# Optimization experiments

Measured on AMD Instinct MI355X. Metric: run time of the kernel, lower is better.

## Reference

```python
import jax, jax.numpy as jnp
import numpy as np

N_NODES = 100000
N_EDGES = 1600000
N_FEAT = 128
HIDDEN = 128
N_CLASSES = 40
MAX_DEPTH = 4
INIT_TEMP = 1.0  # temperature (non-trainable)
N_AGGR = 3       # ['mean', 'max', 'self']


def setup_inputs() -> dict:
    key = jax.random.key(0)
    ks = jax.random.split(key, 16)
    s = 1.0 / np.sqrt(HIDDEN)
    inp = {
        'x': jax.random.normal(ks[0], (N_NODES, N_FEAT), dtype=jnp.float32),
        'edge_index': jax.random.randint(ks[1], (2, N_EDGES), 0, N_NODES, dtype=jnp.int32),
        'W_pre': jax.random.normal(ks[2], (N_FEAT, HIDDEN), dtype=jnp.float32) / np.sqrt(N_FEAT),
        'b_pre': jnp.zeros((HIDDEN,), dtype=jnp.float32),
        'W_depth': jax.random.normal(ks[3], (HIDDEN, 2), dtype=jnp.float32) * s,
        'b_depth': jnp.zeros((2,), dtype=jnp.float32),
        'W_aggr': jax.random.normal(ks[4], (HIDDEN, N_AGGR), dtype=jnp.float32) * s,
        'b_aggr': jnp.zeros((N_AGGR,), dtype=jnp.float32),
        'W_conv': jax.random.normal(ks[5], (MAX_DEPTH, HIDDEN, HIDDEN), dtype=jnp.float32) * s,
        'b_conv': jnp.zeros((MAX_DEPTH, HIDDEN), dtype=jnp.float32),
        'W_post': jax.random.normal(ks[6], (HIDDEN, N_CLASSES), dtype=jnp.float32) * s,
        'b_post': jnp.zeros((N_CLASSES,), dtype=jnp.float32),
    }
    return inp


def _mix_aggr_conv(x, src, dst, deg, W, b, aggr_w):
    # MixAggrConvLayer: transform then per-node convex mix of {mean, max, self}
    h = x @ W + b                                   # [N, H]
    msg = h[src]                                    # [E, H] gather
    mean_a = jax.ops.segment_sum(msg, dst, num_segments=N_NODES) / deg[:, None]
    max_a = jax.ops.segment_max(msg, dst, num_segments=N_NODES)
    max_a = jnp.where(jnp.isfinite(max_a), max_a, 0.0)  # isolated nodes -> 0
    return aggr_w[:, 0:1] * mean_a + aggr_w[:, 1:2] * max_a + aggr_w[:, 2:3] * h


def reference(x, edge_index, W_pre, b_pre, W_depth, b_depth, W_aggr, b_aggr,
              W_conv, b_conv, W_post, b_post):
    src, dst = edge_index[0], edge_index[1]
    deg = jnp.maximum(
        jax.ops.segment_sum(jnp.ones((src.shape[0],), jnp.float32), dst,
                            num_segments=N_NODES), 1.0)

    # pre_mp + (Dropout eval = identity) + ReLU
    h = jax.nn.relu(x @ W_pre + b_pre)              # [N, H]

    continue_pr = jnp.ones((N_NODES,), jnp.float32)
    selected = jnp.zeros((N_NODES, HIDDEN), jnp.float32)
    for i in range(MAX_DEPTH):
        hd = jax.lax.stop_gradient(h)               # controllers see detached x
        stop_prob = jax.nn.softmax((hd @ W_depth + b_depth) / INIT_TEMP, axis=-1)
        aggr_prob = jax.nn.softmax((hd @ W_aggr + b_aggr) / INIT_TEMP, axis=-1)
        h = _mix_aggr_conv(h, src, dst, deg, W_conv[i], b_conv[i], aggr_prob)
        h = jax.nn.relu(h)                          # dropout (eval) + relu
        selected = selected + (continue_pr * stop_prob[:, 1])[:, None] * h
        continue_pr = continue_pr * stop_prob[:, 0]

    logits = selected @ W_post + b_post             # [N, C]
    return jax.nn.log_softmax(logits, axis=1)
```

## Files before the change

### kernel.cpp

```cpp
#include <hip/hip_runtime.h>
#include <math.h>

#define HIDDEN 128
#define NCLS 40
#define BMAX 1024

typedef __attribute__((ext_vector_type(8))) short short8;
typedef __attribute__((ext_vector_type(4))) float f32x4;
typedef __attribute__((ext_vector_type(2))) float f32x2;

__device__ __forceinline__ unsigned short f2bf(float f) {
    unsigned u = __float_as_uint(f);
    unsigned r = u + 0x7FFFu + ((u >> 16) & 1u);
    return (unsigned short)(r >> 16);
}
__device__ __forceinline__ float bf_lo(unsigned u) { return __uint_as_float(u << 16); }
__device__ __forceinline__ float bf_hi(unsigned u) { return __uint_as_float(u & 0xFFFF0000u); }

__global__ void k_wprep(const float* __restrict__ Wp, const float* __restrict__ Wc,
                        const float* __restrict__ Wd, const float* __restrict__ Wa,
                        unsigned short* __restrict__ WpreT, unsigned short* __restrict__ WT) {
    int i = blockIdx.x * 256 + threadIdx.x;
    if (i < 16384) {
        int n = i >> 7, k = i & 127;
        WpreT[i] = f2bf(Wp[k * 128 + n]);
    } else if (i < 16384 + 4 * 18432) {
        int j = i - 16384;
        int d = j / 18432;
        int rem = j % 18432;
        int n = rem >> 7, k = rem & 127;
        float v = 0.f;
        if (n < 128)      v = Wc[d * 16384 + k * 128 + n];
        else if (n < 130) v = Wd[k * 2 + (n - 128)];
        else if (n < 133) v = Wa[k * 3 + (n - 130)];
        WT[j] = f2bf(v);
    }
}


__launch_bounds__(256)
__global__ void k_bcount(const int* __restrict__ ei, int E, int* __restrict__ bucket_cnt) {
    __shared__ int hist[BMAX];
    const int tid = threadIdx.x;
    for (int i = tid; i < BMAX; i += 256) hist[i] = 0;
    __syncthreads();
    const int e0 = blockIdx.x * 4096;
    #pragma unroll
    for (int i = 0; i < 16; i++) {
        int e = e0 + i * 256 + tid;
        if (e < E) atomicAdd(&hist[ei[E + e] >> 8], 1);
    }
    __syncthreads();
    for (int i = tid; i < BMAX; i += 256) {
        int v = hist[i];
        if (v > 0) atomicAdd(&bucket_cnt[i], v);
    }
}

__global__ void k_bscan(const int* __restrict__ bucket_cnt, int nb,
                        int* __restrict__ bucket_base, int* __restrict__ bucket_cursor) {
    __shared__ int sd[256];
    const int tid = threadIdx.x;
    int v[4];
    int sum = 0;
    #pragma unroll
    for (int j = 0; j < 4; j++) {
        int b = tid * 4 + j;
        v[j] = (b < nb) ? bucket_cnt[b] : 0;
        sum += v[j];
    }
    sd[tid] = sum;
    __syncthreads();
    #pragma unroll
    for (int off = 1; off < 256; off <<= 1) {
        int t = (tid >= off) ? sd[tid - off] : 0;
        __syncthreads();
        sd[tid] += t;
        __syncthreads();
    }
    int base = sd[tid] - sum;
    #pragma unroll
    for (int j = 0; j < 4; j++) {
        int b = tid * 4 + j;
        if (b < nb) {
            bucket_base[b] = base;
            bucket_cursor[b] = base;
            base += v[j];
        }
    }
}

__launch_bounds__(256)
__global__ void k_bin(const int* __restrict__ ei, int E,
                      int* __restrict__ bucket_cursor, unsigned* __restrict__ binned) {
    __shared__ int hist[BMAX];
    __shared__ int rankc[BMAX];
    __shared__ int lbase[BMAX];
    const int tid = threadIdx.x;
    const int e0 = blockIdx.x * 4096;
    for (int i = tid; i < BMAX; i += 256) { hist[i] = 0; rankc[i] = 0; }
    __syncthreads();
    int bkt[16];
    unsigned pk[16];
    #pragma unroll
    for (int i = 0; i < 16; i++) {
        int e = e0 + i * 256 + tid;
        if (e < E) {
            int s = ei[e];
            int d = ei[E + e];
            bkt[i] = d >> 8;
            pk[i] = ((unsigned)(d & 255) << 24) | (unsigned)s;
            atomicAdd(&hist[bkt[i]], 1);
        } else bkt[i] = -1;
    }
    __syncthreads();
    for (int i = tid; i < BMAX; i += 256)
        if (hist[i] > 0) lbase[i] = atomicAdd(&bucket_cursor[i], hist[i]);
    __syncthreads();
    #pragma unroll
    for (int i = 0; i < 16; i++) {
        if (bkt[i] >= 0) {
            int r = atomicAdd(&rankc[bkt[i]], 1);
            binned[lbase[bkt[i]] + r] = pk[i];
        }
    }
}

__launch_bounds__(256)
__global__ void k_scatter(const unsigned* __restrict__ binned,
                          const int* __restrict__ bucket_base,
                          const int* __restrict__ bucket_cnt,
                          int* __restrict__ row_start,
                          int* __restrict__ csr_off, int N) {
    __shared__ int hist[256];
    __shared__ int rs[256];
    __shared__ int cur[256];
    const int tid = threadIdx.x;
    hist[tid] = 0;
    __syncthreads();
    const int base = bucket_base[blockIdx.x];
    const int cnt = bucket_cnt[blockIdx.x];
    for (int i = tid; i < cnt; i += 256)
        atomicAdd(&hist[binned[base + i] >> 24], 1);
    __syncthreads();
    int v = hist[tid];
    rs[tid] = v;
    __syncthreads();
    #pragma unroll
    for (int off = 1; off < 256; off <<= 1) {
        int t = (tid >= off) ? rs[tid - off] : 0;
        __syncthreads();
        rs[tid] += t;
        __syncthreads();
    }
    int gstart = base + rs[tid] - v;
    int n = (blockIdx.x << 8) + tid;
    if (n < N) {
        row_start[n] = gstart;
        if (n == N - 1) row_start[N] = gstart + v;
    }
    __syncthreads();
    rs[tid] = gstart;
    cur[tid] = 0;
    __syncthreads();
    for (int i = tid; i < cnt; i += 256) {
        unsigned p = binned[base + i];
        int dl = (int)(p >> 24);
        int r = atomicAdd(&cur[dl], 1);
        csr_off[rs[dl] + r] = (int)((p & 0xFFFFFFu) << 7);
    }
}


template <bool AF32, bool CTRL>
__launch_bounds__(256)
__global__ void k_gemm_mfma(const void* __restrict__ Ain,
                            const unsigned short* __restrict__ Wt,
                            const float* __restrict__ bias,
                            unsigned short* __restrict__ Cb,
                            unsigned char* __restrict__ C8,
                            float* __restrict__ ctrl,
                            int M, int do_relu) {
    __shared__ unsigned short Ws[144 * 132];
    const int tid = threadIdx.x;
    const int lane = tid & 63;
    const int wv = tid >> 6;
    const int row_blk = blockIdx.x * 128;
    const int rows0 = wv * 32;
    const int l15 = lane & 15;
    const int q = lane >> 4;
    const int RWS = CTRL ? 144 : 128;

    for (int c = tid; c < RWS * 16; c += 256) {
        int r = c >> 4, ch = c & 15;
        *(uint4*)&Ws[r * 132 + ch * 8] = *(const uint4*)(Wt + (size_t)r * HIDDEN + ch * 8);
    }
    __syncthreads();

    f32x4 acc[2][8] = {};
    f32x4 acc5[2] = {};
    for (int k0 = 0; k0 < 128; k0 += 32) {
        short8 af[2];
        #pragma unroll
        for (int mi = 0; mi < 2; mi++) {
            int ar = row_blk + rows0 + mi * 16 + l15;
            if (AF32) {
                const float* A = (const float*)Ain;
                float4 v0 = make_float4(0.f, 0.f, 0.f, 0.f);
                float4 v1 = make_float4(0.f, 0.f, 0.f, 0.f);
                if (ar < M) {
                    v0 = *(const float4*)(A + (size_t)ar * HIDDEN + k0 + q * 8);
                    v1 = *(const float4*)(A + (size_t)ar * HIDDEN + k0 + q * 8 + 4);
                }
                short8 t;
                t[0] = (short)f2bf(v0.x); t[1] = (short)f2bf(v0.y);
                t[2] = (short)f2bf(v0.z); t[3] = (short)f2bf(v0.w);
                t[4] = (short)f2bf(v1.x); t[5] = (short)f2bf(v1.y);
                t[6] = (short)f2bf(v1.z); t[7] = (short)f2bf(v1.w);
                af[mi] = t;
            } else {
                const unsigned short* A = (const unsigned short*)Ain;
                short8 t = {};
                if (ar < M) t = *(const short8*)(A + (size_t)ar * HIDDEN + k0 + q * 8);
                af[mi] = t;
            }
        }
        #pragma unroll
        for (int ni = 0; ni < 8; ni++) {
            short8 bw = *(const short8*)&Ws[(ni * 16 + l15) * 132 + k0 + q * 8];
            #pragma unroll
            for (int mi = 0; mi < 2; mi++)
                acc[mi][ni] = __builtin_amdgcn_mfma_f32_16x16x32_bf16(
                    bw, af[mi], acc[mi][ni], 0, 0, 0);
        }
        if (CTRL) {
            short8 bc = *(const short8*)&Ws[(128 + l15) * 132 + k0 + q * 8];
            #pragma unroll
            for (int mi = 0; mi < 2; mi++)
                acc5[mi] = __builtin_amdgcn_mfma_f32_16x16x32_bf16(
                    bc, af[mi], acc5[mi], 0, 0, 0);
        }
    }
    #pragma unroll
    for (int mi = 0; mi < 2; mi++) {
        int node = row_blk + rows0 + mi * 16 + l15;
        if (node < M) {
            #pragma unroll
            for (int ni = 0; ni < 8; ni++) {
                int fb = ni * 16 + q * 4;
                float4 bv = *(const float4*)&bias[fb];
                float o0 = acc[mi][ni][0] + bv.x;
                float o1 = acc[mi][ni][1] + bv.y;
                float o2 = acc[mi][ni][2] + bv.z;
                float o3 = acc[mi][ni][3] + bv.w;
                if (do_relu) {
                    o0 = fmaxf(o0, 0.f); o1 = fmaxf(o1, 0.f);
                    o2 = fmaxf(o2, 0.f); o3 = fmaxf(o3, 0.f);
                }
                unsigned plo, phi;
                asm("v_cvt_pk_bf16_f32 %0, %1, %2" : "=v"(plo) : "v"(o0), "v"(o1));
                asm("v_cvt_pk_bf16_f32 %0, %1, %2" : "=v"(phi) : "v"(o2), "v"(o3));
                uint2 ov;
                ov.x = plo; ov.y = phi;
                *(uint2*)(Cb + (size_t)node * HIDDEN + fb) = ov;
                if (CTRL) {
                    unsigned w8 = 0;
                    w8 = __builtin_amdgcn_cvt_pk_fp8_f32(o0, o1, w8, 0);
                    w8 = __builtin_amdgcn_cvt_pk_fp8_f32(o2, o3, w8, 1);
                    *(unsigned*)(C8 + (size_t)node * HIDDEN + fb) = w8;
                }
            }
            if (CTRL) {
                if (q == 0) {
                    *(float4*)(ctrl + (size_t)node * 8) =
                        make_float4(acc5[mi][0], acc5[mi][1], acc5[mi][2], acc5[mi][3]);
                } else if (q == 1) {
                    ctrl[(size_t)node * 8 + 4] = acc5[mi][0];
                }
            }
        }
    }
}


#define LDE(K, JJ)                                                            \
    unsigned u##K = *(const unsigned short*)(                                 \
        ht8 + (unsigned)__builtin_amdgcn_readlane(soff, (JJ) + K) + lane2);
#define ACE(K)                                                                \
    { f32x2 p_ = __builtin_amdgcn_cvt_pk_f32_fp8(u##K, 0);                    \
      sacc += p_;                                                             \
      mx0 = fmaxf(mx0, p_.x); mx1 = fmaxf(mx1, p_.y); }

__launch_bounds__(256)
__global__ void k_depth(const unsigned char* __restrict__ ht8,
                        const unsigned short* __restrict__ ht,
                        unsigned short* __restrict__ h_out,
                        float* __restrict__ cp, float* __restrict__ wsel,
                        const float* __restrict__ ctrl,
                        const int* __restrict__ row_start,
                        const int* __restrict__ csr_off,
                        const float* __restrict__ bd, const float* __restrict__ ba,
                        int N, int first) {
    const int lane = threadIdx.x & 63;
    const int wave = threadIdx.x >> 6;
    const int node = blockIdx.x * 4 + wave;
    if (node >= N) return;
    const int nodeu = __builtin_amdgcn_readfirstlane(node);
    const int lane2 = lane << 1;

    const int start = row_start[nodeu];
    const int cnt = row_start[nodeu + 1] - start;

    int soff = (lane < cnt) ? csr_off[start + lane] : 0;
    unsigned su = *(const unsigned*)((const char*)ht + ((size_t)nodeu << 8) + (lane << 2));
    float4 c4 = *(const float4*)(ctrl + (size_t)nodeu * 8);
    float cl4 = ctrl[(size_t)nodeu * 8 + 4];

    float d0 = c4.x + bd[0], d1 = c4.y + bd[1];
    float a0 = c4.z + ba[0], a1 = c4.w + ba[1], a2 = cl4 + ba[2];
    float m2 = fmaxf(d0, d1);
    float e0 = __expf(d0 - m2), e1 = __expf(d1 - m2);
    float inv2 = __builtin_amdgcn_rcpf(e0 + e1);
    float sp0 = e0 * inv2, sp1 = e1 * inv2;
    float m3 = fmaxf(fmaxf(a0, a1), a2);
    float f0 = __expf(a0 - m3), f1 = __expf(a1 - m3), f2 = __expf(a2 - m3);
    float inv3 = __builtin_amdgcn_rcpf(f0 + f1 + f2);
    float ap0 = f0 * inv3, ap1 = f1 * inv3, ap2 = f2 * inv3;

    f32x2 sacc = {0.f, 0.f};
    float mx0 = -3.4e38f, mx1 = -3.4e38f;

    for (int eb = 0; eb < cnt; eb += 64) {
        if (eb) {
            int i2 = eb + lane;
            soff = (i2 < cnt) ? csr_off[start + i2] : 0;
        }
        int lim = min(64, cnt - eb);
        int j = 0;
        for (; j + 16 <= lim; j += 16) {
            LDE(0, j)  LDE(1, j)  LDE(2, j)  LDE(3, j)
            LDE(4, j)  LDE(5, j)  LDE(6, j)  LDE(7, j)
            LDE(8, j)  LDE(9, j)  LDE(10, j) LDE(11, j)
            LDE(12, j) LDE(13, j) LDE(14, j) LDE(15, j)
            ACE(0)  ACE(1)  ACE(2)  ACE(3)
            ACE(4)  ACE(5)  ACE(6)  ACE(7)
            ACE(8)  ACE(9)  ACE(10) ACE(11)
            ACE(12) ACE(13) ACE(14) ACE(15)
        }
        if (j + 8 <= lim) {
            LDE(0, j) LDE(1, j) LDE(2, j) LDE(3, j)
            LDE(4, j) LDE(5, j) LDE(6, j) LDE(7, j)
            ACE(0) ACE(1) ACE(2) ACE(3)
            ACE(4) ACE(5) ACE(6) ACE(7)
            j += 8;
        }
        if (j + 4 <= lim) {
            LDE(0, j) LDE(1, j) LDE(2, j) LDE(3, j)
            ACE(0) ACE(1) ACE(2) ACE(3)
            j += 4;
        }
        for (; j < lim; j++) {
            LDE(0, j)
            ACE(0)
        }
    }

    if (cnt == 0) { mx0 = 0.f; mx1 = 0.f; }
    float invd = __builtin_amdgcn_rcpf(fmaxf((float)cnt, 1.0f));
    float h0 = ap0 * (sacc.x * invd) + ap1 * mx0 + ap2 * bf_lo(su);
    float h1 = ap0 * (sacc.y * invd) + ap1 * mx1 + ap2 * bf_hi(su);
    h0 = fmaxf(h0, 0.f);
    h1 = fmaxf(h1, 0.f);
    unsigned po = ((unsigned)f2bf(h1) << 16) | (unsigned)f2bf(h0);
    *(unsigned*)((char*)h_out + ((size_t)nodeu << 8) + (lane << 2)) = po;

    if (lane == 0) {
        float cpv = first ? 1.0f : cp[nodeu];
        wsel[nodeu] = cpv * sp1;
        cp[nodeu] = cpv * sp0;
    }
}


__launch_bounds__(256)
__global__ void k_post(const unsigned short* __restrict__ h_all, size_t hstride,
                       const float* __restrict__ wsel, int N,
                       const float* __restrict__ Wp, const float* __restrict__ bp,
                       float* __restrict__ out) {
    __shared__ float Ss[32][132];
    __shared__ float Wt[NCLS][132];
    __shared__ float bs[NCLS];
    const int tid = threadIdx.x;
    const int n0 = blockIdx.x * 32;

    for (int i = tid; i < (HIDDEN * NCLS) / 4; i += 256) {
        float4 v = *(const float4*)&Wp[i * 4];
        int f = i * 4;
        int k = f / NCLS, c = f % NCLS;
        float e[4] = {v.x, v.y, v.z, v.w};
        #pragma unroll
        for (int j = 0; j < 4; j++) {
            int cc = c + j, kk = k;
            if (cc >= NCLS) { cc -= NCLS; kk++; }
            Wt[cc][kk] = e[j];
        }
    }
    if (tid < NCLS) bs[tid] = bp[tid];

    const int node_l = tid >> 3;
    const int kc = (tid & 7) * 16;
    const int ng = n0 + node_l;
    float sel[16];
    #pragma unroll
    for (int i = 0; i < 16; i++) sel[i] = 0.f;
    if (ng < N) {
        #pragma unroll
        for (int d = 0; d < 4; d++) {
            float w = wsel[(size_t)d * N + ng];
            const unsigned short* hrow = h_all + (size_t)(d + 1) * hstride + (size_t)ng * HIDDEN;
            #pragma unroll
            for (int u = 0; u < 2; u++) {
                uint4 p = *(const uint4*)(hrow + kc + u * 8);
                unsigned vs[4] = {p.x, p.y, p.z, p.w};
                #pragma unroll
                for (int j = 0; j < 4; j++) {
                    sel[u * 8 + j * 2 + 0] += w * bf_lo(vs[j]);
                    sel[u * 8 + j * 2 + 1] += w * bf_hi(vs[j]);
                }
            }
        }
    }
    #pragma unroll
    for (int u = 0; u < 4; u++)
        *(float4*)&Ss[node_l][kc + u * 4] =
            make_float4(sel[u * 4], sel[u * 4 + 1], sel[u * 4 + 2], sel[u * 4 + 3]);
    __syncthreads();

    const int c0 = (tid & 7) * 5;
    float z[5];
    #pragma unroll
    for (int i = 0; i < 5; i++) z[i] = bs[c0 + i];
    for (int k = 0; k < HIDDEN; k += 4) {
        float4 s4 = *(const float4*)&Ss[node_l][k];
        #pragma unroll
        for (int i = 0; i < 5; i++) {
            float4 w4 = *(const float4*)&Wt[c0 + i][k];
            z[i] += s4.x * w4.x + s4.y * w4.y + s4.z * w4.z + s4.w * w4.w;
        }
    }
    float m = z[0];
    #pragma unroll
    for (int i = 1; i < 5; i++) m = fmaxf(m, z[i]);
    #pragma unroll
    for (int off = 1; off < 8; off <<= 1) m = fmaxf(m, __shfl_xor(m, off));
    float s = 0.f;
    #pragma unroll
    for (int i = 0; i < 5; i++) s += expf(z[i] - m);
    #pragma unroll
    for (int off = 1; off < 8; off <<= 1) s += __shfl_xor(s, off);
    float lg = m + logf(s);
    if (ng < N) {
        #pragma unroll
        for (int i = 0; i < 5; i++)
            out[(size_t)ng * NCLS + c0 + i] = z[i] - lg;
    }
}


extern "C" void kernel_launch(void* const* d_in, const int* in_sizes, int n_in,
                              void* d_out, int out_size, void* d_ws, size_t ws_size,
                              hipStream_t stream) {
    const float* x      = (const float*)d_in[0];
    const int*   ei     = (const int*)d_in[1];
    const float* W_pre  = (const float*)d_in[2];
    const float* b_pre  = (const float*)d_in[3];
    const float* W_dep  = (const float*)d_in[4];
    const float* b_dep  = (const float*)d_in[5];
    const float* W_aggr = (const float*)d_in[6];
    const float* b_aggr = (const float*)d_in[7];
    const float* W_conv = (const float*)d_in[8];
    const float* b_conv = (const float*)d_in[9];
    const float* W_post = (const float*)d_in[10];
    const float* b_post = (const float*)d_in[11];

    const int N = in_sizes[0] / HIDDEN;
    const int E = in_sizes[1] / 2;
    const int nbuckets = (N + 255) >> 8;

    char* ws = (char*)d_ws;
    size_t off = 0;
    auto alloc = [&](size_t bytes) -> void* {
        void* p = ws + off;
        off += (bytes + 255) & ~(size_t)255;
        return p;
    };
    const size_t hstride = (size_t)N * HIDDEN;
    unsigned short* h_all  = (unsigned short*)alloc(5 * hstride * 2);
    unsigned short* ht     = (unsigned short*)alloc(hstride * 2);
    unsigned char*  ht8    = (unsigned char*)alloc(hstride);
    float* cp       = (float*)alloc((size_t)N * 4);
    float* wsel     = (float*)alloc((size_t)4 * N * 4);
    float* ctrl     = (float*)alloc((size_t)N * 8 * 4);
    unsigned short* WpreT = (unsigned short*)alloc(128 * 128 * 2);
    unsigned short* WT    = (unsigned short*)alloc(4 * 144 * 128 * 2);
    int*   row_start= (int*)alloc((size_t)(N + 8) * 4);
    int*   bucket_cnt    = (int*)alloc(BMAX * 4);
    int*   bucket_base   = (int*)alloc(BMAX * 4);
    int*   bucket_cursor = (int*)alloc(BMAX * 4);
    int*   csr_off  = (int*)alloc((size_t)E * 4);
    unsigned* binned = (unsigned*)alloc((size_t)E * 4);

    hipMemsetAsync(bucket_cnt, 0, BMAX * 4, stream);

    int ebb = (E + 4095) / 4096;
    k_bcount<<<ebb, 256, 0, stream>>>(ei, E, bucket_cnt);
    k_bscan<<<1, 256, 0, stream>>>(bucket_cnt, nbuckets, bucket_base, bucket_cursor);
    k_bin<<<ebb, 256, 0, stream>>>(ei, E, bucket_cursor, binned);
    k_scatter<<<nbuckets, 256, 0, stream>>>(binned, bucket_base, bucket_cnt,
                                            row_start, csr_off, N);

    int wtot = 16384 + 4 * 18432;
    k_wprep<<<(wtot + 255) / 256, 256, 0, stream>>>(W_pre, W_conv, W_dep, W_aggr,
                                                    WpreT, WT);

    int gblk = (N + 127) / 128;
    k_gemm_mfma<true, false><<<gblk, 256, 0, stream>>>(x, WpreT, b_pre, h_all,
                                                       nullptr, nullptr, N, 1);

    int nb4 = (N + 3) / 4;
    for (int d = 0; d < 4; d++) {
        unsigned short* h_d  = h_all + (size_t)d * hstride;
        unsigned short* h_n  = h_all + (size_t)(d + 1) * hstride;
        k_gemm_mfma<false, true><<<gblk, 256, 0, stream>>>(h_d, WT + (size_t)d * 18432,
                                                           b_conv + (size_t)d * HIDDEN,
                                                           ht, ht8, ctrl, N, 0);
        k_depth<<<nb4, 256, 0, stream>>>(ht8, ht, h_n, cp, wsel + (size_t)d * N, ctrl,
                                         row_start, csr_off,
                                         b_dep, b_aggr, N, d == 0 ? 1 : 0);
    }
    k_post<<<(N + 31) / 32, 256, 0, stream>>>(h_all, hstride, wsel, N,
                                              W_post, b_post, (float*)d_out);
}
```

Measured before the change: 528.1 us.

## Split wave into two half-waves gathering 4 fp8 features per lane

The edge-gather loop in k_depth now has each half-wave handle a different neighbour edge, with each lane loading 4 fp8 features (32-bit) instead of 2 (16-bit). This halves the number of load instructions per edge and widens each memory access. Partial sums and maxes are then merged across halves with xor-32 shuffles. It also uses the hardware v_cvt_pk_bf16_f32 instruction for the bf16 output conversion, and only the lower half-wave writes the result.

```diff
diff --git a/kernel.cpp b/kernel.cpp
--- a/kernel.cpp
+++ b/kernel.cpp
@@ -283,13 +283,16 @@
 }
 
 
-#define LDE(K, JJ)                                                            \
-    unsigned u##K = *(const unsigned short*)(                                 \
-        ht8 + (unsigned)__builtin_amdgcn_readlane(soff, (JJ) + K) + lane2);
-#define ACE(K)                                                                \
-    { f32x2 p_ = __builtin_amdgcn_cvt_pk_f32_fp8(u##K, 0);                    \
-      sacc += p_;                                                             \
-      mx0 = fmaxf(mx0, p_.x); mx1 = fmaxf(mx1, p_.y); }
+#define LDP(K, JJ)                                                            \
+    int sa##K = __builtin_amdgcn_readlane(soff, (JJ) + 2 * K);                \
+    int sb##K = __builtin_amdgcn_readlane(soff, (JJ) + 2 * K + 1);            \
+    unsigned u##K = *(const unsigned*)(ht8 + (unsigned)(half ? sb##K : sa##K) + fb4);
+#define ACP(K)                                                                \
+    { f32x2 plo_ = __builtin_amdgcn_cvt_pk_f32_fp8(u##K, 0);                  \
+      f32x2 phi_ = __builtin_amdgcn_cvt_pk_f32_fp8(u##K, 1);                  \
+      s01 += plo_; s23 += phi_;                                               \
+      mx0 = fmaxf(mx0, plo_.x); mx1 = fmaxf(mx1, plo_.y);                     \
+      mx2 = fmaxf(mx2, phi_.x); mx3 = fmaxf(mx3, phi_.y); }
 
 __launch_bounds__(256)
 __global__ void k_depth(const unsigned char* __restrict__ ht8,
@@ -306,13 +309,14 @@
     const int node = blockIdx.x * 4 + wave;
     if (node >= N) return;
     const int nodeu = __builtin_amdgcn_readfirstlane(node);
-    const int lane2 = lane << 1;
+    const int half = lane >> 5;
+    const unsigned fb4 = (unsigned)((lane & 31) << 2);
 
     const int start = row_start[nodeu];
     const int cnt = row_start[nodeu + 1] - start;
 
     int soff = (lane < cnt) ? csr_off[start + lane] : 0;
-    unsigned su = *(const unsigned*)((const char*)ht + ((size_t)nodeu << 8) + (lane << 2));
+    uint2 su = *(const uint2*)((const char*)ht + ((size_t)nodeu << 8) + ((lane & 31) << 3));
     float4 c4 = *(const float4*)(ctrl + (size_t)nodeu * 8);
     float cl4 = ctrl[(size_t)nodeu * 8 + 4];
 
@@ -327,8 +331,8 @@
     float inv3 = __builtin_amdgcn_rcpf(f0 + f1 + f2);
     float ap0 = f0 * inv3, ap1 = f1 * inv3, ap2 = f2 * inv3;
 
-    f32x2 sacc = {0.f, 0.f};
-    float mx0 = -3.4e38f, mx1 = -3.4e38f;
+    f32x2 s01 = {0.f, 0.f}, s23 = {0.f, 0.f};
+    float mx0 = -3.4e38f, mx1 = -3.4e38f, mx2 = -3.4e38f, mx3 = -3.4e38f;
 
     for (int eb = 0; eb < cnt; eb += 64) {
         if (eb) {
@@ -338,42 +342,59 @@
         int lim = min(64, cnt - eb);
         int j = 0;
         for (; j + 16 <= lim; j += 16) {
-            LDE(0, j)  LDE(1, j)  LDE(2, j)  LDE(3, j)
-            LDE(4, j)  LDE(5, j)  LDE(6, j)  LDE(7, j)
-            LDE(8, j)  LDE(9, j)  LDE(10, j) LDE(11, j)
-            LDE(12, j) LDE(13, j) LDE(14, j) LDE(15, j)
-            ACE(0)  ACE(1)  ACE(2)  ACE(3)
-            ACE(4)  ACE(5)  ACE(6)  ACE(7)
-            ACE(8)  ACE(9)  ACE(10) ACE(11)
-            ACE(12) ACE(13) ACE(14) ACE(15)
+            LDP(0, j) LDP(1, j) LDP(2, j) LDP(3, j)
+            LDP(4, j) LDP(5, j) LDP(6, j) LDP(7, j)
+            ACP(0) ACP(1) ACP(2) ACP(3)
+            ACP(4) ACP(5) ACP(6) ACP(7)
         }
         if (j + 8 <= lim) {
-            LDE(0, j) LDE(1, j) LDE(2, j) LDE(3, j)
-            LDE(4, j) LDE(5, j) LDE(6, j) LDE(7, j)
-            ACE(0) ACE(1) ACE(2) ACE(3)
-            ACE(4) ACE(5) ACE(6) ACE(7)
+            LDP(0, j) LDP(1, j) LDP(2, j) LDP(3, j)
+            ACP(0) ACP(1) ACP(2) ACP(3)
             j += 8;
         }
         if (j + 4 <= lim) {
-            LDE(0, j) LDE(1, j) LDE(2, j) LDE(3, j)
-            ACE(0) ACE(1) ACE(2) ACE(3)
+            LDP(0, j) LDP(1, j)
+            ACP(0) ACP(1)
             j += 4;
         }
-        for (; j < lim; j++) {
-            LDE(0, j)
-            ACE(0)
-        }
-    }
-
-    if (cnt == 0) { mx0 = 0.f; mx1 = 0.f; }
+        if (j + 2 <= lim) {
+            LDP(0, j)
+            ACP(0)
+            j += 2;
+        }
+        if (j < lim) {
+            int sa = __builtin_amdgcn_readlane(soff, j);
+            if (half == 0) {
+                unsigned u = *(const unsigned*)(ht8 + (unsigned)sa + fb4);
+                f32x2 plo_ = __builtin_amdgcn_cvt_pk_f32_fp8(u, 0);
+                f32x2 phi_ = __builtin_amdgcn_cvt_pk_f32_fp8(u, 1);
+                s01 += plo_; s23 += phi_;
+                mx0 = fmaxf(mx0, plo_.x); mx1 = fmaxf(mx1, plo_.y);
+                mx2 = fmaxf(mx2, phi_.x); mx3 = fmaxf(mx3, phi_.y);
+            }
+        }
+    }
+
+    s01.x += __shfl_xor(s01.x, 32); s01.y += __shfl_xor(s01.y, 32);
+    s23.x += __shfl_xor(s23.x, 32); s23.y += __shfl_xor(s23.y, 32);
+    mx0 = fmaxf(mx0, __shfl_xor(mx0, 32)); mx1 = fmaxf(mx1, __shfl_xor(mx1, 32));
+    mx2 = fmaxf(mx2, __shfl_xor(mx2, 32)); mx3 = fmaxf(mx3, __shfl_xor(mx3, 32));
+
+    if (cnt == 0) { mx0 = 0.f; mx1 = 0.f; mx2 = 0.f; mx3 = 0.f; }
     float invd = __builtin_amdgcn_rcpf(fmaxf((float)cnt, 1.0f));
-    float h0 = ap0 * (sacc.x * invd) + ap1 * mx0 + ap2 * bf_lo(su);
-    float h1 = ap0 * (sacc.y * invd) + ap1 * mx1 + ap2 * bf_hi(su);
-    h0 = fmaxf(h0, 0.f);
-    h1 = fmaxf(h1, 0.f);
-    unsigned po = ((unsigned)f2bf(h1) << 16) | (unsigned)f2bf(h0);
-    *(unsigned*)((char*)h_out + ((size_t)nodeu << 8) + (lane << 2)) = po;
-
+    float h0 = ap0 * (s01.x * invd) + ap1 * mx0 + ap2 * bf_lo(su.x);
+    float h1 = ap0 * (s01.y * invd) + ap1 * mx1 + ap2 * bf_hi(su.x);
+    float h2 = ap0 * (s23.x * invd) + ap1 * mx2 + ap2 * bf_lo(su.y);
+    float h3 = ap0 * (s23.y * invd) + ap1 * mx3 + ap2 * bf_hi(su.y);
+    h0 = fmaxf(h0, 0.f); h1 = fmaxf(h1, 0.f);
+    h2 = fmaxf(h2, 0.f); h3 = fmaxf(h3, 0.f);
+    unsigned plo, phi;
+    asm("v_cvt_pk_bf16_f32 %0, %1, %2" : "=v"(plo) : "v"(h0), "v"(h1));
+    asm("v_cvt_pk_bf16_f32 %0, %1, %2" : "=v"(phi) : "v"(h2), "v"(h3));
+    if (half == 0) {
+        uint2 ov; ov.x = plo; ov.y = phi;
+        *(uint2*)((char*)h_out + ((size_t)nodeu << 8) + ((lane & 31) << 3)) = ov;
+    }
     if (lane == 0) {
         float cpv = first ? 1.0f : cp[nodeu];
         wsel[nodeu] = cpv * sp1;
```

After: 534.6 us. No clear change (+1.2%).
